# Kernel optimization log

Hardware: AMD Instinct MI355X
Metric: run time of the kernel (lower is better)

The kernel has to match this reference:

```python
import jax, jax.numpy as jnp
import numpy as np

EMBED_DIM = 1024
NUM_HEADS = 16
HEAD_DIM = EMBED_DIM // NUM_HEADS
LORA_R = 128
LORA_SCALING = 1.0 / LORA_R  # loralib default lora_alpha=1


def setup_inputs() -> dict:
    key = jax.random.key(0)
    k1, k2, k3, k4 = jax.random.split(key, 4)
    B, S, E = 2, 2048, EMBED_DIM
    x = jax.random.normal(k1, (B, S, E), dtype=jnp.float32)
    # in_proj: LoRA linear 3E -> 3E (see notes), bias-free
    W_in = jax.random.normal(k2, (3 * E, 3 * E), dtype=jnp.float32) * (1.0 / np.sqrt(3 * E))
    A_in = jax.random.normal(k3, (LORA_R, 3 * E), dtype=jnp.float32) * (1.0 / np.sqrt(3 * E))
    B_in = jnp.zeros((3 * E, LORA_R), dtype=jnp.float32)  # loralib inits B to zero
    W_out = jax.random.normal(k4, (E, E), dtype=jnp.float32) * (1.0 / np.sqrt(E))
    return {"x": x, "W_in": W_in, "A_in": A_in, "B_in": B_in, "W_out": W_out}


def reference(x, W_in, A_in, B_in, W_out):
    B, S, E = x.shape
    H, D = NUM_HEADS, HEAD_DIM
    x3 = jnp.concatenate([x, x, x], axis=-1)  # [B,S,3E]
    # LoRA linear: x3 @ W^T + (x3 @ A^T) @ B^T * scaling
    qkv = x3 @ W_in.T + ((x3 @ A_in.T) @ B_in.T) * LORA_SCALING  # [B,S,3E]
    Q, K, V = jnp.split(qkv, 3, axis=-1)
    # [B,S,E] -> [B,H,S,D]
    Q = Q.reshape(B, S, H, D).transpose(0, 2, 1, 3)
    K = K.reshape(B, S, H, D).transpose(0, 2, 1, 3)
    V = V.reshape(B, S, H, D).transpose(0, 2, 1, 3)
    scores = jnp.einsum("bhqd,bhkd->bhqk", Q, K) / jnp.sqrt(jnp.float32(D))
    attn = jax.nn.softmax(scores, axis=-1)
    out = jnp.einsum("bhqk,bhkd->bhqd", attn, V)  # [B,H,S,D]
    out = out.transpose(0, 2, 1, 3).reshape(B, S, E)
    return out @ W_out.T
```

## Files before the change

### kernel.cpp

```cpp
#include <hip/hip_runtime.h>

#define E_DIM 1024
#define H_NUM 16
#define D_HEAD 64
#define SEQ 2048
#define BATCH 2
#define NTOK 4096
#define R_LORA 128
#define Q3 3072

#if __has_builtin(__builtin_amdgcn_exp2f)
#define K_PRESCALE (0.125f * 1.44269504088896f)
#define FAST_EXP(x) __builtin_amdgcn_exp2f(x)
#else
#define K_PRESCALE 0.125f
#define FAST_EXP(x) __expf(x)
#endif

typedef float floatx4 __attribute__((ext_vector_type(4)));
typedef __bf16 bf16x8 __attribute__((ext_vector_type(8)));
typedef __bf16 bf16x4 __attribute__((ext_vector_type(4)));
typedef bf16x8 bf16x8_al __attribute__((may_alias));
typedef bf16x4 bf16x4_al __attribute__((may_alias));

__device__ __forceinline__ void async_cp16(const void* g, void* l) {
  __builtin_amdgcn_global_load_lds(
      (__attribute__((address_space(1))) unsigned int*)(size_t)g,
      (__attribute__((address_space(3))) unsigned int*)l, 16, 0, 0);
}

__device__ __forceinline__ void wg_barrier() {
  asm volatile("" ::: "memory");
  __builtin_amdgcn_s_barrier();
  asm volatile("" ::: "memory");
}

__global__ __launch_bounds__(256) void prep_all(const float* __restrict__ x,
                                                const float* __restrict__ Wi,
                                                const float* __restrict__ Bl,
                                                const float* __restrict__ Ai,
                                                const float* __restrict__ Wo,
                                                __bf16* __restrict__ xb,
                                                __bf16* __restrict__ wtot,
                                                __bf16* __restrict__ binb,
                                                __bf16* __restrict__ aeffT,
                                                __bf16* __restrict__ wob) {
  __shared__ __bf16 tile[64][65];
  const int blk = blockIdx.x, t = threadIdx.x;
  if (blk < 4096) {
    int idx = (blk * 256 + t) * 4;
    float4 v = *(const float4*)(x + idx);
    bf16x4 o = {(__bf16)v.x, (__bf16)v.y, (__bf16)v.z, (__bf16)v.w};
    *(bf16x4_al*)(xb + idx) = o;
  } else if (blk < 7168) {
    int j = blk - 4096, e = t * 4;
    const float* r = Wi + (size_t)j * Q3;
    float4 a = *(const float4*)(r + e);
    float4 b = *(const float4*)(r + e + 1024);
    float4 c = *(const float4*)(r + e + 2048);
    bf16x4 o = {(__bf16)(a.x + b.x + c.x), (__bf16)(a.y + b.y + c.y),
                (__bf16)(a.z + b.z + c.z), (__bf16)(a.w + b.w + c.w)};
    *(bf16x4_al*)(wtot + (size_t)j * E_DIM + e) = o;
  } else if (blk < 7552) {
    int idx = (blk - 7168) * 256 + t;
    int j = idx >> 5, cq = (idx & 31) * 4;
    float4 v = *(const float4*)(Bl + (size_t)j * R_LORA + cq);
    bf16x4 o = {(__bf16)v.x, (__bf16)v.y, (__bf16)v.z, (__bf16)v.w};
    *(bf16x4_al*)(binb + (size_t)j * R_LORA + cq) = o;
  } else if (blk < 7584) {
    int b2 = blk - 7552;
    int r0 = (b2 & 1) * 64, e0 = (b2 >> 1) * 64;
    int c = t & 63, r4 = t >> 6;
#pragma unroll
    for (int i = 0; i < 16; i++) {
      int row = r4 + i * 4;
      const float* rp = Ai + (size_t)(r0 + row) * Q3 + e0 + c;
      tile[row][c] = (__bf16)(rp[0] + rp[1024] + rp[2048]);
    }
    __syncthreads();
#pragma unroll
    for (int i = 0; i < 16; i++) {
      int er = r4 + i * 4;
      aeffT[(size_t)(e0 + er) * R_LORA + r0 + c] = tile[c][er];
    }
  } else {
    int idx = ((blk - 7584) * 256 + t) * 4;
    float4 v = *(const float4*)(Wo + idx);
    bf16x4 o = {(__bf16)v.x, (__bf16)v.y, (__bf16)v.z, (__bf16)v.w};
    *(bf16x4_al*)(wob + idx) = o;
  }
}

template <int KTOT, int LDA, int LDB, int EPI>
__global__ __launch_bounds__(256) void gemm_mfma(const __bf16* A, const __bf16* Bm,
                                                 float* fOut, __bf16* o0, __bf16* o1,
                                                 __bf16* o2) {
  __shared__ __bf16 lds[24576];
  const int t = threadIdx.x;
  const int wave = t >> 6, lane = t & 63;
  const int wm = wave & 1, wn = wave >> 1;
  const int lr = lane & 15, lq = lane >> 4;
  const int m0 = blockIdx.x * 128, n0 = blockIdx.y * 128;

  floatx4 acc[4][4] = {};
  const __bf16* gA = A + (size_t)(m0 + lr) * LDA + lq * 8;
  const __bf16* gB = Bm + (size_t)(n0 + lr) * LDB + lq * 8;

  auto STAGE = [&](int kk, int bb) {
    async_cp16(gA + (size_t)(wave * 16) * LDA + kk, lds + bb + wave * 512);
    async_cp16(gA + (size_t)((wave + 4) * 16) * LDA + kk, lds + bb + (wave + 4) * 512);
    async_cp16(gB + (size_t)(wave * 16) * LDB + kk, lds + bb + 4096 + wave * 512);
    async_cp16(gB + (size_t)((wave + 4) * 16) * LDB + kk, lds + bb + 4096 + (wave + 4) * 512);
  };

  STAGE(0, 0);
  STAGE(32, 8192);
  int cur = 0, tgt = 16384;

  for (int kk = 0; kk < KTOT; kk += 32) {
    wg_barrier();
    if (kk + 64 < KTOT) {
      STAGE(kk + 64, tgt);
      asm volatile("s_waitcnt vmcnt(8)" ::: "memory");
    } else if (kk + 32 < KTOT) {
      asm volatile("s_waitcnt vmcnt(4)" ::: "memory");
    } else {
      asm volatile("s_waitcnt vmcnt(0)" ::: "memory");
    }
    wg_barrier();
    const int cb = cur;
    bf16x8 af[4], bfr[4];
#pragma unroll
    for (int i = 0; i < 4; i++)
      af[i] = *(const bf16x8_al*)(lds + cb + (wm * 4 + i) * 512 + lane * 8);
#pragma unroll
    for (int j = 0; j < 4; j++)
      bfr[j] = *(const bf16x8_al*)(lds + cb + 4096 + (wn * 4 + j) * 512 + lane * 8);
#pragma unroll
    for (int i = 0; i < 4; i++)
#pragma unroll
      for (int j = 0; j < 4; j++)
        acc[i][j] = __builtin_amdgcn_mfma_f32_16x16x32_bf16(af[i], bfr[j], acc[i][j], 0, 0, 0);
    cur += 8192; if (cur == 24576) cur = 0;
    tgt += 8192; if (tgt == 24576) tgt = 0;
  }

#pragma unroll
  for (int i = 0; i < 4; i++)
#pragma unroll
    for (int j = 0; j < 4; j++) {
      const int row0 = m0 + wm * 64 + i * 16 + lq * 4;
      const int col = n0 + wn * 64 + j * 16 + lr;
      if (EPI == 0) {
#pragma unroll
        for (int r = 0; r < 4; r++)
          fOut[(size_t)(row0 + r) * 1024 + col] = acc[i][j][r];
      } else if (EPI == 3) {
#pragma unroll
        for (int r = 0; r < 4; r++) {
          size_t off = (size_t)(row0 + r) * 1024 + col;
          o0[off] = (__bf16)((float)o0[off] + acc[i][j][r] * (1.0f / 128.0f));
        }
      } else {
        int part = col >> 10, e = col & 1023, h = e >> 6, d = e & 63;
        int b = row0 >> 11, s = row0 & 2047;
        if (part == 2) {
          bf16x4 pv;
#pragma unroll
          for (int r = 0; r < 4; r++) pv[r] = (__bf16)acc[i][j][r];
          *(bf16x4_al*)(o2 + ((size_t)(b * H_NUM + h) * D_HEAD + d) * SEQ + s) = pv;
        } else {
#pragma unroll
          for (int r = 0; r < 4; r++) {
            float v = acc[i][j][r];
            if (part == 1) v *= K_PRESCALE;
            size_t off = ((size_t)(b * H_NUM + h) * SEQ + (s + r)) * D_HEAD + d;
            (part == 0 ? o0 : o1)[off] = (__bf16)v;
          }
        }
      }
    }
}

__global__ __launch_bounds__(256, 2) void attn_kernel(const __bf16* __restrict__ Q,
                                                      const __bf16* __restrict__ K,
                                                      const __bf16* __restrict__ Vt,
                                                      __bf16* __restrict__ O) {
  __shared__ __bf16 smem[40960];
  const int t = threadIdx.x, wave = t >> 6, lane = t & 63;
  const int lr = lane & 15, lq = lane >> 4;
  const int lin = blockIdx.x;
  const int xcd = lin & 7, ix = lin >> 3;
  const int bh = xcd * 4 + (ix >> 4);
  const int q0 = (ix & 15) * 128;
  __bf16* plsw = smem + 32768 + wave * 2048;
  const size_t hbase = (size_t)bh * SEQ * D_HEAD;
  const __bf16* Kp = K + hbase;
  const __bf16* vtb = Vt + (size_t)bh * D_HEAD * SEQ;
  const int row7 = lr & 7;

  bf16x8 qf[2][2];
#pragma unroll
  for (int qg = 0; qg < 2; qg++) {
    const __bf16* qp = Q + hbase + (size_t)(q0 + wave * 32 + qg * 16 + lr) * D_HEAD + lq * 8;
    qf[qg][0] = *(const bf16x8_al*)qp;
    qf[qg][1] = *(const bf16x8_al*)(qp + 32);
  }
  asm volatile("" : "+v"(qf[0][0]), "+v"(qf[0][1]), "+v"(qf[1][0]), "+v"(qf[1][1]));

  floatx4 oacc[2][4] = {};
  float lsum[2] = {0.0f, 0.0f};

  auto STAGE = [&](int ktb, int bb) {
#pragma unroll
    for (int ii = 0; ii < 8; ii++) {
      int sg = wave * 8 + ii;
      const __bf16* src;
      if (sg < 16) {
        src = Kp + (size_t)(ktb + (sg >> 1) * 16 + lr) * D_HEAD + (sg & 1) * 32 + lq * 8;
      } else {
        int v = sg - 16;
        src = vtb + (size_t)((v >> 2) * 16 + lr) * SEQ + ktb + (v & 3) * 32 + lq * 8;
      }
      async_cp16(src, smem + bb + sg * 512);
    }
  };

  STAGE(0, 0);

  const int NT = SEQ / 128;
  for (int it = 0; it < NT; ++it) {
    const int cur = (it & 1) ? 16384 : 0;
    wg_barrier();
    if (it + 1 < NT) {
      STAGE((it + 1) * 128, 16384 - cur);
      asm volatile("s_waitcnt vmcnt(8)" ::: "memory");
    } else {
      asm volatile("s_waitcnt vmcnt(0)" ::: "memory");
    }
    wg_barrier();
    const __bf16* kls = smem + cur;
    const __bf16* vls = smem + cur + 8192;

#pragma unroll
    for (int h = 0; h < 2; h++) {
#pragma unroll
      for (int kb = 0; kb < 4; kb++) {
        bf16x8 kf0 = *(const bf16x8_al*)(kls + (h * 8 + kb * 2) * 512 + lane * 8);
        bf16x8 kf1 = *(const bf16x8_al*)(kls + (h * 8 + kb * 2 + 1) * 512 + lane * 8);
#pragma unroll
        for (int qg = 0; qg < 2; qg++) {
          floatx4 sv = {};
          __builtin_amdgcn_s_setprio(1);
          sv = __builtin_amdgcn_mfma_f32_16x16x32_bf16(kf0, qf[qg][0], sv, 0, 0, 0);
          sv = __builtin_amdgcn_mfma_f32_16x16x32_bf16(kf1, qf[qg][1], sv, 0, 0, 0);
          __builtin_amdgcn_s_setprio(0);
          bf16x4 pv;
#pragma unroll
          for (int r = 0; r < 4; r++) {
            float p = FAST_EXP(sv[r]);
            lsum[qg] += p;
            pv[r] = (__bf16)p;
          }
          int chunk = (kb * 2 + (lq >> 1)) ^ row7;
          *(bf16x4_al*)(plsw + qg * 1024 + lr * 64 + chunk * 8 + (lq & 1) * 4) = pv;
        }
      }

#pragma unroll
      for (int kc = 0; kc < 2; kc++) {
        bf16x8 vf[4];
#pragma unroll
        for (int jd = 0; jd < 4; jd++)
          vf[jd] = *(const bf16x8_al*)(vls + (jd * 4 + h * 2 + kc) * 512 + lane * 8);
        int chunk = (kc * 4 + lq) ^ row7;
#pragma unroll
        for (int qg = 0; qg < 2; qg++) {
          bf16x8 pf = *(const bf16x8_al*)(plsw + qg * 1024 + lr * 64 + chunk * 8);
          __builtin_amdgcn_s_setprio(1);
#pragma unroll
          for (int jd = 0; jd < 4; jd++)
            oacc[qg][jd] = __builtin_amdgcn_mfma_f32_16x16x32_bf16(pf, vf[jd], oacc[qg][jd], 0, 0, 0);
          __builtin_amdgcn_s_setprio(0);
        }
      }
    }
  }

#pragma unroll
  for (int qg = 0; qg < 2; qg++) {
    lsum[qg] += __shfl_xor(lsum[qg], 16);
    lsum[qg] += __shfl_xor(lsum[qg], 32);
  }

  const int b = bh >> 4, hh = bh & 15;
#pragma unroll
  for (int qg = 0; qg < 2; qg++)
#pragma unroll
    for (int r = 0; r < 4; r++) {
      float linv = 1.0f / __shfl(lsum[qg], lq * 4 + r);
      int s = q0 + wave * 32 + qg * 16 + lq * 4 + r;
#pragma unroll
      for (int jd = 0; jd < 4; jd++) {
        int d = jd * 16 + lr;
        O[((size_t)b * SEQ + s) * E_DIM + hh * D_HEAD + d] = (__bf16)(oacc[qg][jd][r] * linv);
      }
    }
}

extern "C" void kernel_launch(void* const* d_in, const int* in_sizes, int n_in,
                              void* d_out, int out_size, void* d_ws, size_t ws_size,
                              hipStream_t stream) {
  const float* x  = (const float*)d_in[0];
  const float* Wi = (const float*)d_in[1];
  const float* Ai = (const float*)d_in[2];
  const float* Bi = (const float*)d_in[3];
  const float* Wo = (const float*)d_in[4];
  float* out = (float*)d_out;
  char* ws = (char*)d_ws;

  __bf16* xb    = (__bf16*)(ws);
  __bf16* wtot  = (__bf16*)(ws + 8388608);
  __bf16* binb  = (__bf16*)(ws + 14680064);
  __bf16* aeffT = (__bf16*)(ws + 15466496);
  __bf16* wob   = (__bf16*)(ws + 15728640);
  __bf16* qh    = (__bf16*)(ws + 17825792);
  __bf16* kh    = (__bf16*)(ws + 26214400);
  __bf16* vt    = (__bf16*)(ws + 34603008);
  __bf16* oh    = (__bf16*)(ws + 42991616);

  prep_all<<<8608, 256, 0, stream>>>(x, Wi, Bi, Ai, Wo, xb, wtot, binb, aeffT, wob);

  gemm_mfma<128, 128, 128, 3><<<dim3(24, 8), 256, 0, stream>>>(
      binb, aeffT, nullptr, wtot, nullptr, nullptr);
  gemm_mfma<1024, 1024, 1024, 1><<<dim3(32, 24), 256, 0, stream>>>(
      xb, wtot, nullptr, qh, kh, vt);
  attn_kernel<<<dim3(512), 256, 0, stream>>>(qh, kh, vt, oh);
  gemm_mfma<1024, 1024, 1024, 0><<<dim3(32, 8), 256, 0, stream>>>(
      oh, wob, out, nullptr, nullptr, nullptr);
}
```

Measured before the change: 220.1 us.

## Load K and V fragments directly from global memory instead of LDS staging

Removes the double-buffered async LDS staging of K/V tiles and the per-tile workgroup barriers in the attention kernel. Each wave now reads its K and V MFMA fragments straight from global memory, relying on L1/L2 caching. This shrinks LDS to the P scratch area and drops synchronisation, but every wave refetches the same K/V data with no latency hiding from prefetch.

Measured after the change: 290.5 us. 32.0% more time.

```diff
diff --git a/kernel.cpp b/kernel.cpp
--- a/kernel.cpp
+++ b/kernel.cpp
@@ -186,14 +186,14 @@
                                                       const __bf16* __restrict__ K,
                                                       const __bf16* __restrict__ Vt,
                                                       __bf16* __restrict__ O) {
-  __shared__ __bf16 smem[40960];
+  __shared__ __bf16 smem[8192];
   const int t = threadIdx.x, wave = t >> 6, lane = t & 63;
   const int lr = lane & 15, lq = lane >> 4;
   const int lin = blockIdx.x;
   const int xcd = lin & 7, ix = lin >> 3;
   const int bh = xcd * 4 + (ix >> 4);
   const int q0 = (ix & 15) * 128;
-  __bf16* plsw = smem + 32768 + wave * 2048;
+  __bf16* plsw = smem + wave * 2048;
   const size_t hbase = (size_t)bh * SEQ * D_HEAD;
   const __bf16* Kp = K + hbase;
   const __bf16* vtb = Vt + (size_t)bh * D_HEAD * SEQ;
@@ -211,43 +211,14 @@
   floatx4 oacc[2][4] = {};
   float lsum[2] = {0.0f, 0.0f};
 
-  auto STAGE = [&](int ktb, int bb) {
-#pragma unroll
-    for (int ii = 0; ii < 8; ii++) {
-      int sg = wave * 8 + ii;
-      const __bf16* src;
-      if (sg < 16) {
-        src = Kp + (size_t)(ktb + (sg >> 1) * 16 + lr) * D_HEAD + (sg & 1) * 32 + lq * 8;
-      } else {
-        int v = sg - 16;
-        src = vtb + (size_t)((v >> 2) * 16 + lr) * SEQ + ktb + (v & 3) * 32 + lq * 8;
-      }
-      async_cp16(src, smem + bb + sg * 512);
-    }
-  };
-
-  STAGE(0, 0);
-
-  const int NT = SEQ / 128;
-  for (int it = 0; it < NT; ++it) {
-    const int cur = (it & 1) ? 16384 : 0;
-    wg_barrier();
-    if (it + 1 < NT) {
-      STAGE((it + 1) * 128, 16384 - cur);
-      asm volatile("s_waitcnt vmcnt(8)" ::: "memory");
-    } else {
-      asm volatile("s_waitcnt vmcnt(0)" ::: "memory");
-    }
-    wg_barrier();
-    const __bf16* kls = smem + cur;
-    const __bf16* vls = smem + cur + 8192;
-
+  for (int kt = 0; kt < SEQ; kt += 128) {
 #pragma unroll
     for (int h = 0; h < 2; h++) {
 #pragma unroll
       for (int kb = 0; kb < 4; kb++) {
-        bf16x8 kf0 = *(const bf16x8_al*)(kls + (h * 8 + kb * 2) * 512 + lane * 8);
-        bf16x8 kf1 = *(const bf16x8_al*)(kls + (h * 8 + kb * 2 + 1) * 512 + lane * 8);
+        const __bf16* kp0 = Kp + (size_t)(kt + h * 64 + kb * 16 + lr) * D_HEAD + lq * 8;
+        bf16x8 kf0 = *(const bf16x8_al*)kp0;
+        bf16x8 kf1 = *(const bf16x8_al*)(kp0 + 32);
 #pragma unroll
         for (int qg = 0; qg < 2; qg++) {
           floatx4 sv = {};
@@ -272,7 +243,8 @@
         bf16x8 vf[4];
 #pragma unroll
         for (int jd = 0; jd < 4; jd++)
-          vf[jd] = *(const bf16x8_al*)(vls + (jd * 4 + h * 2 + kc) * 512 + lane * 8);
+          vf[jd] = *(const bf16x8_al*)(vtb + (size_t)(jd * 16 + lr) * SEQ + kt +
+                                       (h * 2 + kc) * 32 + lq * 8);
         int chunk = (kc * 4 + lq) ^ row7;
 #pragma unroll
         for (int qg = 0; qg < 2; qg++) {
```

## Use BK=64 double-buffered GEMM tiles with XCD-aware block remapping

Applied to the files above, without the earlier changes.

The GEMM main loop goes from a 3-stage K=32 pipeline to a 2-stage K=64 double buffer. This halves the number of barriers per K and issues 8 async copies per thread per stage. Block indices are also remapped so consecutive linear blocks on the same XCD share M-tile ranges, which should improve L2 reuse on MI355X's multi-XCD layout. The cost is more LDS per block (64KB) and a shallower prefetch depth, which may reduce occupancy and latency hiding.

New measurement: 219.8 us. Within noise of the previous version (-0.1%).

```diff
diff --git a/kernel.cpp b/kernel.cpp
--- a/kernel.cpp
+++ b/kernel.cpp
@@ -95,54 +95,64 @@
 __global__ __launch_bounds__(256) void gemm_mfma(const __bf16* A, const __bf16* Bm,
                                                  float* fOut, __bf16* o0, __bf16* o1,
                                                  __bf16* o2) {
-  __shared__ __bf16 lds[24576];
+  __shared__ __bf16 lds[32768];
   const int t = threadIdx.x;
   const int wave = t >> 6, lane = t & 63;
   const int wm = wave & 1, wn = wave >> 1;
   const int lr = lane & 15, lq = lane >> 4;
-  const int m0 = blockIdx.x * 128, n0 = blockIdx.y * 128;
+  const int lin = blockIdx.y * gridDim.x + blockIdx.x;
+  const int xcd = lin & 7, c = lin >> 3;
+  const int mtpx = gridDim.x >> 3;
+  const int m0 = (xcd * mtpx + c % mtpx) * 128;
+  const int n0 = (c / mtpx) * 128;
 
   floatx4 acc[4][4] = {};
   const __bf16* gA = A + (size_t)(m0 + lr) * LDA + lq * 8;
   const __bf16* gB = Bm + (size_t)(n0 + lr) * LDB + lq * 8;
 
   auto STAGE = [&](int kk, int bb) {
-    async_cp16(gA + (size_t)(wave * 16) * LDA + kk, lds + bb + wave * 512);
-    async_cp16(gA + (size_t)((wave + 4) * 16) * LDA + kk, lds + bb + (wave + 4) * 512);
-    async_cp16(gB + (size_t)(wave * 16) * LDB + kk, lds + bb + 4096 + wave * 512);
-    async_cp16(gB + (size_t)((wave + 4) * 16) * LDB + kk, lds + bb + 4096 + (wave + 4) * 512);
+#pragma unroll
+    for (int ii = 0; ii < 8; ii++) {
+      int sg = wave * 8 + ii;
+      const __bf16* src;
+      if (sg < 16) {
+        src = gA + (size_t)((sg >> 1) * 16) * LDA + kk + (sg & 1) * 32;
+      } else {
+        int v = sg - 16;
+        src = gB + (size_t)((v >> 1) * 16) * LDB + kk + (v & 1) * 32;
+      }
+      async_cp16(src, lds + bb + sg * 512);
+    }
   };
 
   STAGE(0, 0);
-  STAGE(32, 8192);
-  int cur = 0, tgt = 16384;
-
-  for (int kk = 0; kk < KTOT; kk += 32) {
+  int cur = 0;
+
+  for (int kk = 0; kk < KTOT; kk += 64) {
     wg_barrier();
     if (kk + 64 < KTOT) {
-      STAGE(kk + 64, tgt);
+      STAGE(kk + 64, cur ^ 16384);
       asm volatile("s_waitcnt vmcnt(8)" ::: "memory");
-    } else if (kk + 32 < KTOT) {
-      asm volatile("s_waitcnt vmcnt(4)" ::: "memory");
     } else {
       asm volatile("s_waitcnt vmcnt(0)" ::: "memory");
     }
     wg_barrier();
-    const int cb = cur;
-    bf16x8 af[4], bfr[4];
-#pragma unroll
-    for (int i = 0; i < 4; i++)
-      af[i] = *(const bf16x8_al*)(lds + cb + (wm * 4 + i) * 512 + lane * 8);
-#pragma unroll
-    for (int j = 0; j < 4; j++)
-      bfr[j] = *(const bf16x8_al*)(lds + cb + 4096 + (wn * 4 + j) * 512 + lane * 8);
-#pragma unroll
-    for (int i = 0; i < 4; i++)
+#pragma unroll
+    for (int c2 = 0; c2 < 2; c2++) {
+      bf16x8 af[4], bfr[4];
+#pragma unroll
+      for (int i = 0; i < 4; i++)
+        af[i] = *(const bf16x8_al*)(lds + cur + ((wm * 4 + i) * 2 + c2) * 512 + lane * 8);
 #pragma unroll
       for (int j = 0; j < 4; j++)
-        acc[i][j] = __builtin_amdgcn_mfma_f32_16x16x32_bf16(af[i], bfr[j], acc[i][j], 0, 0, 0);
-    cur += 8192; if (cur == 24576) cur = 0;
-    tgt += 8192; if (tgt == 24576) tgt = 0;
+        bfr[j] = *(const bf16x8_al*)(lds + cur + (16 + (wn * 4 + j) * 2 + c2) * 512 + lane * 8);
+#pragma unroll
+      for (int i = 0; i < 4; i++)
+#pragma unroll
+        for (int j = 0; j < 4; j++)
+          acc[i][j] = __builtin_amdgcn_mfma_f32_16x16x32_bf16(af[i], bfr[j], acc[i][j], 0, 0, 0);
+    }
+    cur ^= 16384;
   }
 
 #pragma unroll
```
